# Kernel optimization log

Measured on AMD Instinct MI355X. Metric: run time of the kernel, lower is better.

The kernel has to match this reference:

```python
import jax, jax.numpy as jnp
import numpy as np

NPG = 39      # nodes per graph, from (1+8+64+9)*(39+1)=3280 = lin1 in_features
NEG_SLOPE = 0.2


def gat_conv(x, src, dst, W, a_src, a_dst, b, n):
    """PyG GATConv, heads=1, self-loops already appended to (src, dst).
    x:[N,Fin] W:[Fin,Fout] a_src/a_dst:[Fout] b:[Fout] -> [N,Fout]"""
    h = x @ W                                        # [N,Fout]
    e = jax.nn.leaky_relu(h[src] @ a_src + h[dst] @ a_dst, NEG_SLOPE)  # [E]
    m = jax.lax.stop_gradient(jax.ops.segment_max(e, dst, num_segments=n))
    w = jnp.exp(e - m[dst])
    denom = jax.ops.segment_sum(w, dst, num_segments=n)
    alpha = w / (denom[dst] + 1e-16)                 # segment softmax per target node
    out = jax.ops.segment_sum(alpha[:, None] * h[src], dst, num_segments=n)
    return out + b


def setup_inputs() -> dict:
    key = jax.random.key(0)
    ks = jax.random.split(key, 20)
    B, DEG = 4096, 8
    N = B * NPG
    E = N * DEG
    x = jax.random.normal(ks[0], (N, 1), dtype=jnp.float32)
    # block-diagonal edges: each node emits DEG edges to random nodes in SAME graph
    src = jnp.repeat(jnp.arange(N, dtype=jnp.int64), DEG)
    offs = (src // NPG) * NPG
    dst = offs + jax.random.randint(ks[1], (E,), 0, NPG, dtype=jnp.int64)
    edge_index = jnp.stack([src, dst])
    batch_vec = jnp.repeat(jnp.arange(B, dtype=jnp.int64), NPG)

    def glorot(k, shape):
        fan = shape[0] + (shape[1] if len(shape) > 1 else 1)
        s = jnp.sqrt(6.0 / fan)
        return jax.random.uniform(k, shape, jnp.float32, -s, s)

    p = {
        'W1': glorot(ks[2], (1, 8)),   'a1s': glorot(ks[3], (8,)),  'a1d': glorot(ks[4], (8,)),  'b1': jnp.zeros((8,), jnp.float32),
        'W2': glorot(ks[5], (8, 64)),  'a2s': glorot(ks[6], (64,)), 'a2d': glorot(ks[7], (64,)), 'b2': jnp.zeros((64,), jnp.float32),
        'W3': glorot(ks[8], (64, 9)),  'a3s': glorot(ks[9], (9,)),  'a3d': glorot(ks[10], (9,)), 'b3': jnp.zeros((9,), jnp.float32),
        'lW1': glorot(ks[11], (3280, 5000)), 'lb1': jnp.zeros((5000,), jnp.float32),
        'lW2': glorot(ks[12], (5000, 1024)), 'lb2': jnp.zeros((1024,), jnp.float32),
        'lW3': glorot(ks[13], (1024, 9)),    'lb3': jnp.zeros((9,), jnp.float32),
    }
    return {'x': x, 'edge_index': edge_index, 'batch_vec': batch_vec, **p}


def reference(x, edge_index, batch_vec,
              W1, a1s, a1d, b1, W2, a2s, a2d, b2, W3, a3s, a3d, b3,
              lW1, lb1, lW2, lb2, lW3, lb3):
    N = x.shape[0]
    B = N // NPG
    loops = jnp.arange(N, dtype=edge_index.dtype)
    src = jnp.concatenate([edge_index[0], loops])   # GATConv add_self_loops=True
    dst = jnp.concatenate([edge_index[1], loops])

    res = x.reshape(B, -1)                                    # [B,39]
    out0 = jax.ops.segment_max(x, batch_vec, num_segments=B)  # [B,1]

    h1 = jax.nn.relu(gat_conv(x, src, dst, W1, a1s, a1d, b1, N))   # dropout = eval no-op
    res1 = h1.reshape(B, -1)                                   # [B,312]
    out1 = jax.ops.segment_max(h1, batch_vec, num_segments=B)

    h2 = jax.nn.relu(gat_conv(h1, src, dst, W2, a2s, a2d, b2, N))
    res2 = h2.reshape(B, -1)                                   # [B,2496]
    out2 = jax.ops.segment_max(h2, batch_vec, num_segments=B)

    h3 = jax.nn.relu(gat_conv(h2, src, dst, W3, a3s, a3d, b3, N))
    res3 = h3.reshape(B, -1)                                   # [B,351]
    out3 = jax.ops.segment_max(h3, batch_vec, num_segments=B)

    f = jnp.concatenate([res, res1, res2, res3, out0, out1, out2, out3], axis=1)  # [B,3280]
    f = jax.nn.relu(f @ lW1 + lb1)
    f = jax.nn.relu(f @ lW2 + lb2)
    return f @ lW3 + lb3                                       # [B,9]
```

## Files before the change

kernel.cpp:

```cpp
#include <hip/hip_runtime.h>
#include <hip/hip_bf16.h>
#include <hip/hip_fp16.h>
#include <stdint.h>


typedef float f32x4 __attribute__((ext_vector_type(4)));
typedef short bf16x8 __attribute__((ext_vector_type(8)));
typedef _Float16 f16x8 __attribute__((ext_vector_type(8)));

__device__ __forceinline__ unsigned fenc(float f) {
  int s = __float_as_int(f);
  return s < 0 ? ~(unsigned)s : ((unsigned)s | 0x80000000u);
}
__device__ __forceinline__ float fdec(unsigned u) {
  return (u & 0x80000000u) ? __int_as_float((int)(u & 0x7fffffffu))
                           : __int_as_float(~(int)u);
}

__device__ __forceinline__ void wbar() {
  asm volatile("s_waitcnt lgkmcnt(0)" ::: "memory");
}


__global__ __launch_bounds__(128) void gnn_conv_wpg(
    const float* __restrict__ x,
    const int* __restrict__ esrc, const int* __restrict__ edst,
    const float* __restrict__ W1, const float* __restrict__ a1s, const float* __restrict__ a1d, const float* __restrict__ b1,
    const float* __restrict__ W2, const float* __restrict__ a2s, const float* __restrict__ a2d, const float* __restrict__ b2,
    const float* __restrict__ W3, const float* __restrict__ a3s, const float* __restrict__ a3d, const float* __restrict__ b3,
    __hip_bfloat16* __restrict__ fA,
    const float* __restrict__ lW1, const float* __restrict__ lW2,
    short* __restrict__ W1T, short* __restrict__ W2T)
{
  __shared__ __align__(16) char smem[36768];
  const int tid = threadIdx.x;
  const int bid = blockIdx.x;

  if (bid >= 2048) {
    float (*t)[260] = (float(*)[260])smem;
    const int cid = bid - 2048;
    const float* W; short* WT; int ktile, ntile, K0, N0, KT;
    if (cid < 4160) { W = lW1; WT = W1T; ktile = cid % 208; ntile = cid / 208; K0 = 3280; N0 = 5000; KT = 52; }
    else { int c2 = cid - 4160; W = lW2; WT = W2T; ktile = c2 % 320; ntile = c2 / 320; K0 = 5000; N0 = 1024; KT = 80; }

    const int kb = ktile * 16, nb = ntile * 256;
    const int wv = tid >> 6, lnc = tid & 63;
#pragma unroll
    for (int r = 0; r < 8; ++r) {
      int k = kb + wv * 8 + r;
      int n = nb + lnc * 4;
      f32x4 v = (f32x4){0.f, 0.f, 0.f, 0.f};
      if (k < K0 && n < N0) v = *(const f32x4*)&W[(size_t)k * N0 + n];
      *(f32x4*)&t[wv * 8 + r][lnc * 4] = v;
    }
    __syncthreads();
#pragma unroll
    for (int h = 0; h < 4; ++h) {
      int c = h * 128 + tid;
      int nl = c >> 1, kc = c & 1;
      int n = nb + nl, k = kb + kc * 8;
      union { bf16x8 v; __hip_bfloat16 b[8]; } z;
#pragma unroll
      for (int j = 0; j < 8; ++j) z.b[j] = __float2bfloat16(t[kc * 8 + j][nl]);
      int rt = n >> 7, mi = (n >> 4) & 7, lr = n & 15;
      int kt = k >> 6, kq = (k >> 5) & 1, lc = (k >> 3) & 3;
      size_t addr = ((((size_t)rt * KT) + kt) * 16 + mi * 2 + kq) * 512 + ((size_t)lr + 16 * lc) * 8;
      *(bf16x8*)&WT[addr] = z.v;
    }
    return;
  }

  const int w = tid >> 6, ln = tid & 63;
  const int g = bid * 2 + w;

  float* sW3T  = (float*)(smem);
  float* a2buf = (float*)(smem + 2448);
  float* a3sb  = (float*)(smem + 2960);
  float* a3db  = (float*)(smem + 3008);
  float* b3b   = (float*)(smem + 3056);
  char* sl = smem + 3104 + w * 16832;
  float*    A    = (float*)   (sl);
  __half*   Hh2  = (__half*)  (sl + 6864);
  __half*   h1h  = (__half*)  (sl + 12480);
  float*    HfT  = (float*)   (sl + 13120);
  float*    xbuf = (float*)   (sl + 14720);
  float*    sarr = (float*)   (sl + 14880);
  float*    darr = (float*)   (sl + 15040);
  float*    den  = (float*)   (sl + 15200);
  unsigned* umx  = (unsigned*)(sl + 15360);
  unsigned* cntP = (unsigned*)(sl + 15888);

  const int rt = g >> 7, mi = (g >> 4) & 7, lrow = g & 15;
  const size_t gbase = (size_t)rt * 52 * 8192 + (size_t)(mi * 2) * 512 + (size_t)lrow * 8;
#define COLADDR(c) (gbase + (size_t)((c) >> 6) * 8192 + (size_t)(((c) >> 5) & 1) * 512 \
                    + (size_t)(((c) >> 3) & 3) * 128 + ((c) & 7))

  for (int i = tid; i < 576; i += 128) { int k = i / 9, f3 = i - 9 * k; sW3T[f3 * 68 + k] = W3[i]; }
  a2buf[tid] = (tid < 64) ? a2s[tid] : a2d[tid - 64];
  if (tid < 9) { a3sb[tid] = a3s[tid]; a3db[tid] = a3d[tid]; b3b[tid] = b3[tid]; }
  for (int i = ln; i < 132; i += 64) umx[i] = 0u;
  for (int i = ln; i < 234; i += 64) cntP[i] = 0u;
  if (ln < 40) xbuf[ln] = 0.f;
  if (ln == 39) { sarr[39] = 0.f; darr[39] = 0.f; }
  __syncthreads();

  float xv = 0.f;
  if (ln < 39) { xv = x[g * 39 + ln]; xbuf[ln] = xv; fA[COLADDR(ln)] = __float2bfloat16(xv); }
  float c_s = 0.f, c_d = 0.f;
  const float w1r = W1[ln & 7], b1r = b1[ln & 7];
#pragma unroll
  for (int ff = 0; ff < 8; ++ff) { float wv = W1[ff]; c_s += wv * a1s[ff]; c_d += wv * a1d[ff]; }
  const int eb = g * 312, nb0 = g * 39;
  if (ln < 39) atomicMax(&umx[0], fenc(xv));
#pragma unroll
  for (int it = 0; it < 6; ++it) {
    int e = it * 64 + ln;
    if (e < 351) {
      int ls, ld;
      if (e < 312) { ls = esrc[eb + e] - nb0; ld = edst[eb + e] - nb0; }
      else         { ls = e - 312; ld = ls; }
      atomicAdd(&cntP[ld * 6 + (ls >> 3)], 1u << (4 * (ls & 7)));
    }
  }
  wbar();

  auto denseEW = [&](const float* sv, const float* dv) {
    if (ln < 39) {
      unsigned cw[6];
#pragma unroll
      for (int j = 0; j < 6; ++j) cw[j] = cntP[ln * 6 + j];
      float dval = dv[ln];
      float* Ar = &A[ln * 44];
      float sum = 0.f;
#pragma unroll
      for (int c = 0; c < 10; ++c) {
        f32x4 s4 = *(const f32x4*)&sv[c * 4];
        f32x4 w4;
#pragma unroll
        for (int j = 0; j < 4; ++j) {
          int s = c * 4 + j;
          float e = s4[j] + dval;
          e = (e > 0.f) ? e : 0.2f * e;
          unsigned cc = (cw[s >> 3] >> (4 * (s & 7))) & 0xFu;
          float ex = __expf(e);
          float wv = cc ? (float)cc * ex : 0.f;
          w4[j] = wv; sum += wv;
        }
        *(f32x4*)&Ar[c * 4] = w4;
      }
      den[ln] = 1.f / (sum + 1e-16f);
    }
  };

  if (ln < 39) {
    unsigned cw[6];
#pragma unroll
    for (int j = 0; j < 6; ++j) cw[j] = cntP[ln * 6 + j];
    float dval = xbuf[ln] * c_d;
    float q = 0.f, dsum = 0.f;
#pragma unroll
    for (int c = 0; c < 10; ++c) {
      f32x4 x4 = *(const f32x4*)&xbuf[c * 4];
#pragma unroll
      for (int j = 0; j < 4; ++j) {
        int s = c * 4 + j;
        float xs = x4[j];
        float e = xs * c_s + dval;
        e = (e > 0.f) ? e : 0.2f * e;
        unsigned cc = (cw[s >> 3] >> (4 * (s & 7))) & 0xFu;
        float ex = __expf(e);
        float wv = cc ? (float)cc * ex : 0.f;
        q += wv * xs; dsum += wv;
      }
    }
    sarr[ln] = q * (1.f / (dsum + 1e-16f));
  }
  wbar();
#pragma unroll
  for (int it = 0; it < 5; ++it) {
    int slot = it * 64 + ln;
    if (slot < 312) {
      int i = slot >> 3;
      float v = fmaxf(sarr[i] * w1r + b1r, 0.f);
      h1h[slot] = __float2half(v);
      fA[COLADDR(39 + slot)] = __float2bfloat16(v);
      atomicMax(&umx[1 + (ln & 7)], fenc(v));
    }
  }
  wbar();

  float ht2r[40];
  {
    float w2k[8];
#pragma unroll
    for (int k = 0; k < 8; ++k) w2k[k] = W2[k * 64 + ln];
#pragma unroll
    for (int i = 0; i < 39; ++i) {
      f16x8 hr = *(const f16x8*)&h1h[i * 8];
      float hv = 0.f;
#pragma unroll
      for (int k = 0; k < 8; ++k) hv += (float)hr[k] * w2k[k];
      ht2r[i] = hv;
    }
    ht2r[39] = 0.f;
#pragma unroll
    for (int i = 0; i < 39; ++i) Hh2[i * 72 + ln] = __float2half(ht2r[i]);
  }
  wbar();
#pragma unroll
  for (int rr = 0; rr < 2; ++rr) {
    int t = rr * 64 + ln;
    if (t < 78) {
      int node = (t < 39) ? t : t - 39;
      const float* ab = a2buf + ((t < 39) ? 0 : 64);
      const __half* hr = &Hh2[node * 72];
      float s = 0.f;
#pragma unroll
      for (int c = 0; c < 8; ++c) {
        f16x8 hv = *(const f16x8*)&hr[c * 8];
        f32x4 a0 = *(const f32x4*)&ab[c * 8];
        f32x4 a1 = *(const f32x4*)&ab[c * 8 + 4];
        s += (float)hv[0] * a0.x + (float)hv[1] * a0.y + (float)hv[2] * a0.z + (float)hv[3] * a0.w
           + (float)hv[4] * a1.x + (float)hv[5] * a1.y + (float)hv[6] * a1.z + (float)hv[7] * a1.w;
      }
      if (t < 39) sarr[node] = s; else darr[node] = s;
    }
  }
  wbar();
  denseEW(sarr, darr);
  wbar();
  {
    const float b2r = b2[ln];
    for (int i = 0; i < 39; ++i) {
      float inv = den[i];
      const float* Ar = &A[i * 44];
      float acc = 0.f;
#pragma unroll
      for (int c = 0; c < 10; ++c) {
        f32x4 a4 = *(const f32x4*)&Ar[c * 4];
        acc += a4.x * ht2r[c * 4] + a4.y * ht2r[c * 4 + 1]
             + a4.z * ht2r[c * 4 + 2] + a4.w * ht2r[c * 4 + 3];
      }
      float v = fmaxf(acc * inv + b2r, 0.f);
      Hh2[i * 72 + ln] = __float2half(v);
      fA[COLADDR(351 + i * 64 + ln)] = __float2bfloat16(v);
      atomicMax(&umx[9 + ln], fenc(v));
    }
  }
  wbar();

#pragma unroll
  for (int it = 0; it < 6; ++it) {
    int slot = it * 64 + ln;
    if (slot < 351) {
      int i = slot / 9, f3 = slot - 9 * i;
      const __half* hr = &Hh2[i * 72];
      const float* wr = &sW3T[f3 * 68];
      float acc = 0.f;
#pragma unroll
      for (int c = 0; c < 8; ++c) {
        f16x8 hv = *(const f16x8*)&hr[c * 8];
        f32x4 w0 = *(const f32x4*)&wr[c * 8];
        f32x4 w1 = *(const f32x4*)&wr[c * 8 + 4];
        acc += (float)hv[0] * w0.x + (float)hv[1] * w0.y + (float)hv[2] * w0.z + (float)hv[3] * w0.w
             + (float)hv[4] * w1.x + (float)hv[5] * w1.y + (float)hv[6] * w1.z + (float)hv[7] * w1.w;
      }
      HfT[f3 * 44 + i] = acc;
    }
  }
  if (ln < 9) HfT[ln * 44 + 39] = 0.f;
  wbar();
#pragma unroll
  for (int rr = 0; rr < 2; ++rr) {
    int t = rr * 64 + ln;
    if (t < 78) {
      int node = (t < 39) ? t : t - 39;
      const float* av = (t < 39) ? a3sb : a3db;
      float s = 0.f;
#pragma unroll
      for (int f3 = 0; f3 < 9; ++f3) s += HfT[f3 * 44 + node] * av[f3];
      if (t < 39) sarr[node] = s; else darr[node] = s;
    }
  }
  wbar();
  denseEW(sarr, darr);
  wbar();
#pragma unroll
  for (int it = 0; it < 6; ++it) {
    int slot = it * 64 + ln;
    if (slot < 351) {
      int i = slot / 9, f3 = slot - 9 * i;
      float inv = den[i];
      const float* Ar = &A[i * 44];
      const float* Hr = &HfT[f3 * 44];
      float acc = 0.f;
#pragma unroll
      for (int c = 0; c < 10; ++c) {
        f32x4 a4 = *(const f32x4*)&Ar[c * 4];
        f32x4 h4 = *(const f32x4*)&Hr[c * 4];
        acc += a4.x * h4.x + a4.y * h4.y + a4.z * h4.z + a4.w * h4.w;
      }
      float v = fmaxf(acc * inv + b3b[f3], 0.f);
      fA[COLADDR(2847 + slot)] = __float2bfloat16(v);
      atomicMax(&umx[73 + f3], fenc(v));
    }
  }
  wbar();

#pragma unroll
  for (int it = 0; it < 3; ++it) {
    int idx = it * 64 + ln;
    if (idx < 130) {
      int c = 3198 + idx;
      float v = (idx < 82) ? fdec(umx[idx]) : 0.f;
      fA[COLADDR(c)] = __float2bfloat16(v);
    }
  }
#undef COLADDR
}


__device__ __forceinline__ void gld_lds16(const void* gptr, void* l) {
  typedef const __attribute__((address_space(1))) unsigned int GU;
  typedef __attribute__((address_space(3))) unsigned int LU;
  __builtin_amdgcn_global_load_lds((GU*)gptr, (LU*)l, 16, 0, 0);
}

__global__ __launch_bounds__(256) void gemm_tiled(
    const short* __restrict__ A, const short* __restrict__ B,
    const float* __restrict__ bias, int Nreal,
    void* __restrict__ Cout, int Nn, int KT, int ktPerSplit, int outKT)
{
  __shared__ __align__(16) short lA[8192];
  __shared__ __align__(16) short lB[8192];
  const int tid = threadIdx.x;
  const int w = tid >> 6, L = tid & 63;
  const int lrow = L & 15, lch = L >> 4;
  const int mt = blockIdx.y, nt = blockIdx.x;
  const int mw = (w >> 1) * 4, nw = (w & 1) * 4;
  const int kt0 = blockIdx.z * ktPerSplit, kt1 = kt0 + ktPerSplit;

  const short* Ab = A + ((size_t)mt * KT) * 8192 + (size_t)L * 8;
  const short* Bb = B + ((size_t)nt * KT) * 8192 + (size_t)L * 8;

  f32x4 acc[4][4] = {};

  for (int kt = kt0; kt < kt1; ++kt) {
    const short* Ak = Ab + (size_t)kt * 8192;
    const short* Bk = Bb + (size_t)kt * 8192;
#pragma unroll
    for (int j = 0; j < 4; ++j) {
      int st = w * 4 + j;
      gld_lds16(Ak + st * 512, &lA[st * 512]);
      gld_lds16(Bk + st * 512, &lB[st * 512]);
    }
    __syncthreads();
#pragma unroll
    for (int kk = 0; kk < 2; ++kk) {
      bf16x8 af[4], bfr[4];
#pragma unroll
      for (int i = 0; i < 4; ++i) {
        af[i]  = *(const bf16x8*)&lA[((mw + i) * 2 + kk) * 512 + L * 8];
        bfr[i] = *(const bf16x8*)&lB[((nw + i) * 2 + kk) * 512 + L * 8];
      }
#pragma unroll
      for (int i = 0; i < 4; ++i)
#pragma unroll
        for (int j = 0; j < 4; ++j)
          acc[i][j] = __builtin_amdgcn_mfma_f32_16x16x32_bf16(af[i], bfr[j], acc[i][j], 0, 0, 0);
    }
    __syncthreads();
  }

  __hip_bfloat16* C = (__hip_bfloat16*)Cout;
#pragma unroll
  for (int j = 0; j < 4; ++j) {
    int n = nt * 128 + (nw + j) * 16 + lrow;
    float bn = (n < Nreal) ? bias[n] : 0.f;
    int kt = n >> 6, kq = (n >> 5) & 1, lc2 = (n >> 3) & 3, j2 = n & 7;
#pragma unroll
    for (int i = 0; i < 4; ++i) {
      int mi = mw + i;
      size_t base = ((((size_t)mt * outKT + kt) * 16) + mi * 2 + kq) * 512
                    + (size_t)(lch * 4) * 8 + (size_t)lc2 * 128 + j2;
#pragma unroll
      for (int r = 0; r < 4; ++r)
        C[base + r * 8] = __float2bfloat16(fmaxf(acc[i][j][r] + bn, 0.f));
    }
  }
}

__global__ __launch_bounds__(512) void gemm2_256(
    const short* __restrict__ A, const short* __restrict__ B,
    __half* __restrict__ P)
{
  __shared__ __align__(16) short lA[16384];
  __shared__ __align__(16) short lB[16384];
  const int tid = threadIdx.x;
  const int w = tid >> 6, L = tid & 63;
  const int lrow = L & 15, lch = L >> 4;
  const int wr = w >> 2, wc = w & 3;
  const int nt = blockIdx.x, mt = blockIdx.y, zz = blockIdx.z;
  const int kt0 = zz * 20, kt1 = kt0 + 20;

  const short* A0 = A + ((size_t)(mt * 2) * 80) * 8192;
  const short* A1 = A + ((size_t)(mt * 2 + 1) * 80) * 8192;
  const short* B0 = B + ((size_t)(nt * 2) * 80) * 8192;
  const short* B1 = B + ((size_t)(nt * 2 + 1) * 80) * 8192;

  f32x4 acc[8][4] = {};

  for (int kt = kt0; kt < kt1; ++kt) {
    const size_t ko = (size_t)kt * 8192;
#pragma unroll
    for (int c = 0; c < 2; ++c) {
      int off = (c * 512 + tid) * 8;
      gld_lds16(A0 + ko + off, &lA[off]);
      gld_lds16(A1 + ko + off, &lA[8192 + off]);
      gld_lds16(B0 + ko + off, &lB[off]);
      gld_lds16(B1 + ko + off, &lB[8192 + off]);
    }
    __syncthreads();
#pragma unroll
    for (int kk = 0; kk < 2; ++kk) {
      bf16x8 af[8], bf[4];
#pragma unroll
      for (int i = 0; i < 8; ++i)
        af[i] = *(const bf16x8*)&lA[wr * 8192 + (i * 2 + kk) * 512 + L * 8];
#pragma unroll
      for (int j = 0; j < 4; ++j)
        bf[j] = *(const bf16x8*)&lB[(wc >> 1) * 8192 + (((wc & 1) * 4 + j) * 2 + kk) * 512 + L * 8];
#pragma unroll
      for (int i = 0; i < 8; ++i)
#pragma unroll
        for (int j = 0; j < 4; ++j)
          acc[i][j] = __builtin_amdgcn_mfma_f32_16x16x32_bf16(af[i], bf[j], acc[i][j], 0, 0, 0);
    }
    __syncthreads();
  }

  __half* Pz = P + (size_t)zz * 4096 * 1024;
#pragma unroll
  for (int j = 0; j < 4; ++j) {
    int n = nt * 256 + wc * 64 + j * 16 + lrow;
#pragma unroll
    for (int i = 0; i < 8; ++i)
#pragma unroll
      for (int r = 0; r < 4; ++r) {
        int m = mt * 256 + wr * 128 + i * 16 + lch * 4 + r;
        Pz[(size_t)m * 1024 + n] = __float2half(acc[i][j][r]);
      }
  }
}


__global__ __launch_bounds__(256) void gemm3_fused(
    const __half* __restrict__ P,
    const float* __restrict__ b2v,
    const float* __restrict__ W3,
    const float* __restrict__ b3v,
    float* __restrict__ out)
{
  __shared__ float sW3[9 * 1024];
  int tid = threadIdx.x;
  for (int i = tid; i < 9216; i += 256) { int k = i / 9, j = i - 9 * k; sW3[j * 1024 + k] = W3[i]; }
  __syncthreads();
  int row = blockIdx.x * 4 + (tid >> 6);
  int lane = tid & 63;
  const __half* p0 = P + (size_t)row * 1024;
  const size_t S = (size_t)4096 * 1024;
  float acc[9] = {0, 0, 0, 0, 0, 0, 0, 0, 0};
  for (int t = 0; t < 16; ++t) {
    int k = lane + 64 * t;
    float c = __half2float(p0[k]) + __half2float(p0[k + S])
            + __half2float(p0[k + 2 * S]) + __half2float(p0[k + 3 * S]) + b2v[k];
    c = fmaxf(c, 0.f);
#pragma unroll
    for (int j = 0; j < 9; ++j) acc[j] += c * sW3[j * 1024 + k];
  }
#pragma unroll
  for (int j = 0; j < 9; ++j) {
    float v = acc[j];
    v += __shfl_down(v, 32, 64);
    v += __shfl_down(v, 16, 64);
    v += __shfl_down(v, 8, 64);
    v += __shfl_down(v, 4, 64);
    v += __shfl_down(v, 2, 64);
    v += __shfl_down(v, 1, 64);
    if (lane == 0) out[(size_t)row * 9 + j] = v + b3v[j];
  }
}


extern "C" void kernel_launch(void* const* d_in, const int* in_sizes, int n_in,
                              void* d_out, int out_size, void* d_ws, size_t ws_size,
                              hipStream_t stream)
{
  const float* x   = (const float*)d_in[0];
  const int*   ei  = (const int*)d_in[1];
  const float* W1  = (const float*)d_in[3];
  const float* a1s = (const float*)d_in[4];
  const float* a1d = (const float*)d_in[5];
  const float* b1  = (const float*)d_in[6];
  const float* W2  = (const float*)d_in[7];
  const float* a2s = (const float*)d_in[8];
  const float* a2d = (const float*)d_in[9];
  const float* b2  = (const float*)d_in[10];
  const float* W3  = (const float*)d_in[11];
  const float* a3s = (const float*)d_in[12];
  const float* a3d = (const float*)d_in[13];
  const float* b3  = (const float*)d_in[14];
  const float* lW1 = (const float*)d_in[15];
  const float* lb1 = (const float*)d_in[16];
  const float* lW2 = (const float*)d_in[17];
  const float* lb2 = (const float*)d_in[18];
  const float* lW3 = (const float*)d_in[19];
  const float* lb3 = (const float*)d_in[20];

  const int E = 4096 * 39 * 8;
  const int* esrc = ei;
  const int* edst = ei + E;

  short* fA  = (short*)d_ws;
  short* W1T = fA  + (size_t)4096 * 3328;
  short* C1  = W1T + (size_t)5120 * 3328;
  short* W2T = C1  + (size_t)4096 * 5120;
  __half* P  = (__half*)d_ws;

  gnn_conv_wpg<<<7488, 128, 0, stream>>>(x, esrc, edst,
                                         W1, a1s, a1d, b1, W2, a2s, a2d, b2, W3, a3s, a3d, b3,
                                         (__hip_bfloat16*)fA, lW1, lW2, W1T, W2T);
  gemm_tiled<<<dim3(40, 32, 1), 256, 0, stream>>>(fA, W1T, lb1, 5000, C1, 5120, 52, 52, 80);
  gemm2_256<<<dim3(4, 16, 4), 512, 0, stream>>>(C1, W2T, P);
  gemm3_fused<<<1024, 256, 0, stream>>>(P, lb2, lW3, lb3, (float*)d_out);
}
```

Baseline: 442.4 us.

## Shrink GAT attention buffers to fp16 and retile second GEMM to 128x128 split-K5

The GAT kernel now stores attention weights and layer-3 features in fp16 instead of fp32, pre-scaled to avoid overflow. This cuts per-wave LDS use and may let more blocks fit per CU. The second linear-layer GEMM moves from 256x256 tiles with 4-way split-K to 128x128 tiles with 5-way split-K, giving more blocks and better CU fill. The price is extra partial-sum traffic for the five fp16 partials reduced in the final kernel, plus lower precision in the attention weights.

```diff
diff --git a/kernel.cpp b/kernel.cpp
--- a/kernel.cpp
+++ b/kernel.cpp
@@ -32,7 +32,7 @@
     const float* __restrict__ lW1, const float* __restrict__ lW2,
     short* __restrict__ W1T, short* __restrict__ W2T)
 {
-  __shared__ __align__(16) char smem[36768];
+  __shared__ __align__(16) char smem[29024];
   const int tid = threadIdx.x;
   const int bid = blockIdx.x;
 
@@ -78,17 +78,17 @@
   float* a3sb  = (float*)(smem + 2960);
   float* a3db  = (float*)(smem + 3008);
   float* b3b   = (float*)(smem + 3056);
-  char* sl = smem + 3104 + w * 16832;
-  float*    A    = (float*)   (sl);
-  __half*   Hh2  = (__half*)  (sl + 6864);
-  __half*   h1h  = (__half*)  (sl + 12480);
-  float*    HfT  = (float*)   (sl + 13120);
-  float*    xbuf = (float*)   (sl + 14720);
-  float*    sarr = (float*)   (sl + 14880);
-  float*    darr = (float*)   (sl + 15040);
-  float*    den  = (float*)   (sl + 15200);
-  unsigned* umx  = (unsigned*)(sl + 15360);
-  unsigned* cntP = (unsigned*)(sl + 15888);
+  char* sl = smem + 3104 + w * 12960;
+  __half*   Ah   = (__half*)  (sl);
+  __half*   Hh2  = (__half*)  (sl + 3744);
+  __half*   h1h  = (__half*)  (sl + 9360);
+  __half*   HfT16= (__half*)  (sl + 9984);
+  float*    xbuf = (float*)   (sl + 10848);
+  float*    sarr = (float*)   (sl + 11008);
+  float*    darr = (float*)   (sl + 11168);
+  float*    den  = (float*)   (sl + 11328);
+  unsigned* umx  = (unsigned*)(sl + 11488);
+  unsigned* cntP = (unsigned*)(sl + 12016);
 
   const int rt = g >> 7, mi = (g >> 4) & 7, lrow = g & 15;
   const size_t gbase = (size_t)rt * 52 * 8192 + (size_t)(mi * 2) * 512 + (size_t)lrow * 8;
@@ -130,25 +130,25 @@
 #pragma unroll
       for (int j = 0; j < 6; ++j) cw[j] = cntP[ln * 6 + j];
       float dval = dv[ln];
-      float* Ar = &A[ln * 44];
+      __half* Ar = &Ah[ln * 48];
       float sum = 0.f;
 #pragma unroll
-      for (int c = 0; c < 10; ++c) {
-        f32x4 s4 = *(const f32x4*)&sv[c * 4];
-        f32x4 w4;
-#pragma unroll
-        for (int j = 0; j < 4; ++j) {
-          int s = c * 4 + j;
-          float e = s4[j] + dval;
+      for (int c = 0; c < 5; ++c) {
+        union { f16x8 v; __half h[8]; } z8;
+#pragma unroll
+        for (int j = 0; j < 8; ++j) {
+          int s = c * 8 + j;
+          float e = sv[s] + dval;
           e = (e > 0.f) ? e : 0.2f * e;
           unsigned cc = (cw[s >> 3] >> (4 * (s & 7))) & 0xFu;
-          float ex = __expf(e);
+          float ex = __expf(e) * 0.00390625f;
           float wv = cc ? (float)cc * ex : 0.f;
-          w4[j] = wv; sum += wv;
+          z8.h[j] = __float2half(wv);
+          sum += (float)z8.h[j];
         }
-        *(f32x4*)&Ar[c * 4] = w4;
-      }
-      den[ln] = 1.f / (sum + 1e-16f);
+        *(f16x8*)&Ar[c * 8] = z8.v;
+      }
+      den[ln] = 1.f / (sum + 3.9e-19f);
     }
   };
 
@@ -233,13 +233,13 @@
     const float b2r = b2[ln];
     for (int i = 0; i < 39; ++i) {
       float inv = den[i];
-      const float* Ar = &A[i * 44];
+      const __half* Ar = &Ah[i * 48];
       float acc = 0.f;
 #pragma unroll
-      for (int c = 0; c < 10; ++c) {
-        f32x4 a4 = *(const f32x4*)&Ar[c * 4];
-        acc += a4.x * ht2r[c * 4] + a4.y * ht2r[c * 4 + 1]
-             + a4.z * ht2r[c * 4 + 2] + a4.w * ht2r[c * 4 + 3];
+      for (int c = 0; c < 5; ++c) {
+        f16x8 a8 = *(const f16x8*)&Ar[c * 8];
+#pragma unroll
+        for (int j = 0; j < 8; ++j) acc += (float)a8[j] * ht2r[c * 8 + j];
       }
       float v = fmaxf(acc * inv + b2r, 0.f);
       Hh2[i * 72 + ln] = __float2half(v);
@@ -265,10 +265,10 @@
         acc += (float)hv[0] * w0.x + (float)hv[1] * w0.y + (float)hv[2] * w0.z + (float)hv[3] * w0.w
              + (float)hv[4] * w1.x + (float)hv[5] * w1.y + (float)hv[6] * w1.z + (float)hv[7] * w1.w;
       }
-      HfT[f3 * 44 + i] = acc;
-    }
-  }
-  if (ln < 9) HfT[ln * 44 + 39] = 0.f;
+      HfT16[f3 * 48 + i] = __float2half(acc);
+    }
+  }
+  if (ln < 9) HfT16[ln * 48 + 39] = __float2half(0.f);
   wbar();
 #pragma unroll
   for (int rr = 0; rr < 2; ++rr) {
@@ -278,7 +278,7 @@
       const float* av = (t < 39) ? a3sb : a3db;
       float s = 0.f;
 #pragma unroll
-      for (int f3 = 0; f3 < 9; ++f3) s += HfT[f3 * 44 + node] * av[f3];
+      for (int f3 = 0; f3 < 9; ++f3) s += (float)HfT16[f3 * 48 + node] * av[f3];
       if (t < 39) sarr[node] = s; else darr[node] = s;
     }
   }
@@ -291,14 +291,15 @@
     if (slot < 351) {
       int i = slot / 9, f3 = slot - 9 * i;
       float inv = den[i];
-      const float* Ar = &A[i * 44];
-      const float* Hr = &HfT[f3 * 44];
+      const __half* Ar = &Ah[i * 48];
+      const __half* Hr = &HfT16[f3 * 48];
       float acc = 0.f;
 #pragma unroll
-      for (int c = 0; c < 10; ++c) {
-        f32x4 a4 = *(const f32x4*)&Ar[c * 4];
-        f32x4 h4 = *(const f32x4*)&Hr[c * 4];
-        acc += a4.x * h4.x + a4.y * h4.y + a4.z * h4.z + a4.w * h4.w;
+      for (int c = 0; c < 5; ++c) {
+        f16x8 a8 = *(const f16x8*)&Ar[c * 8];
+        f16x8 h8 = *(const f16x8*)&Hr[c * 8];
+#pragma unroll
+        for (int j = 0; j < 8; ++j) acc += (float)a8[j] * (float)h8[j];
       }
       float v = fmaxf(acc * inv + b3b[f3], 0.f);
       fA[COLADDR(2847 + slot)] = __float2bfloat16(v);
@@ -390,51 +391,47 @@
   }
 }
 
-__global__ __launch_bounds__(512) void gemm2_256(
+__global__ __launch_bounds__(256) void gemm2_128(
     const short* __restrict__ A, const short* __restrict__ B,
     __half* __restrict__ P)
 {
-  __shared__ __align__(16) short lA[16384];
-  __shared__ __align__(16) short lB[16384];
+  __shared__ __align__(16) short lA[8192];
+  __shared__ __align__(16) short lB[8192];
   const int tid = threadIdx.x;
   const int w = tid >> 6, L = tid & 63;
   const int lrow = L & 15, lch = L >> 4;
-  const int wr = w >> 2, wc = w & 3;
-  const int nt = blockIdx.x, mt = blockIdx.y, zz = blockIdx.z;
-  const int kt0 = zz * 20, kt1 = kt0 + 20;
-
-  const short* A0 = A + ((size_t)(mt * 2) * 80) * 8192;
-  const short* A1 = A + ((size_t)(mt * 2 + 1) * 80) * 8192;
-  const short* B0 = B + ((size_t)(nt * 2) * 80) * 8192;
-  const short* B1 = B + ((size_t)(nt * 2 + 1) * 80) * 8192;
-
-  f32x4 acc[8][4] = {};
+  const int mt = blockIdx.y, nt = blockIdx.x, zz = blockIdx.z;
+  const int mw = (w >> 1) * 4, nw = (w & 1) * 4;
+  const int kt0 = zz * 16, kt1 = kt0 + 16;
+
+  const short* Ab = A + ((size_t)mt * 80) * 8192 + (size_t)L * 8;
+  const short* Bb = B + ((size_t)nt * 80) * 8192 + (size_t)L * 8;
+
+  f32x4 acc[4][4] = {};
 
   for (int kt = kt0; kt < kt1; ++kt) {
-    const size_t ko = (size_t)kt * 8192;
-#pragma unroll
-    for (int c = 0; c < 2; ++c) {
-      int off = (c * 512 + tid) * 8;
-      gld_lds16(A0 + ko + off, &lA[off]);
-      gld_lds16(A1 + ko + off, &lA[8192 + off]);
-      gld_lds16(B0 + ko + off, &lB[off]);
-      gld_lds16(B1 + ko + off, &lB[8192 + off]);
+    const short* Ak = Ab + (size_t)kt * 8192;
+    const short* Bk = Bb + (size_t)kt * 8192;
+#pragma unroll
+    for (int j = 0; j < 4; ++j) {
+      int st = w * 4 + j;
+      gld_lds16(Ak + st * 512, &lA[st * 512]);
+      gld_lds16(Bk + st * 512, &lB[st * 512]);
     }
     __syncthreads();
 #pragma unroll
     for (int kk = 0; kk < 2; ++kk) {
-      bf16x8 af[8], bf[4];
-#pragma unroll
-      for (int i = 0; i < 8; ++i)
-        af[i] = *(const bf16x8*)&lA[wr * 8192 + (i * 2 + kk) * 512 + L * 8];
-#pragma unroll
-      for (int j = 0; j < 4; ++j)
-        bf[j] = *(const bf16x8*)&lB[(wc >> 1) * 8192 + (((wc & 1) * 4 + j) * 2 + kk) * 512 + L * 8];
-#pragma unroll
-      for (int i = 0; i < 8; ++i)
+      bf16x8 af[4], bfr[4];
+#pragma unroll
+      for (int i = 0; i < 4; ++i) {
+        af[i]  = *(const bf16x8*)&lA[((mw + i) * 2 + kk) * 512 + L * 8];
+        bfr[i] = *(const bf16x8*)&lB[((nw + i) * 2 + kk) * 512 + L * 8];
+      }
+#pragma unroll
+      for (int i = 0; i < 4; ++i)
 #pragma unroll
         for (int j = 0; j < 4; ++j)
-          acc[i][j] = __builtin_amdgcn_mfma_f32_16x16x32_bf16(af[i], bf[j], acc[i][j], 0, 0, 0);
+          acc[i][j] = __builtin_amdgcn_mfma_f32_16x16x32_bf16(af[i], bfr[j], acc[i][j], 0, 0, 0);
     }
     __syncthreads();
   }
@@ -442,12 +439,12 @@
   __half* Pz = P + (size_t)zz * 4096 * 1024;
 #pragma unroll
   for (int j = 0; j < 4; ++j) {
-    int n = nt * 256 + wc * 64 + j * 16 + lrow;
-#pragma unroll
-    for (int i = 0; i < 8; ++i)
+    int n = nt * 128 + (nw + j) * 16 + lrow;
+#pragma unroll
+    for (int i = 0; i < 4; ++i)
 #pragma unroll
       for (int r = 0; r < 4; ++r) {
-        int m = mt * 256 + wr * 128 + i * 16 + lch * 4 + r;
+        int m = mt * 128 + (mw + i) * 16 + lch * 4 + r;
         Pz[(size_t)m * 1024 + n] = __float2half(acc[i][j][r]);
       }
   }
@@ -472,8 +469,9 @@
   float acc[9] = {0, 0, 0, 0, 0, 0, 0, 0, 0};
   for (int t = 0; t < 16; ++t) {
     int k = lane + 64 * t;
-    float c = __half2float(p0[k]) + __half2float(p0[k + S])
-            + __half2float(p0[k + 2 * S]) + __half2float(p0[k + 3 * S]) + b2v[k];
+    float c = b2v[k];
+#pragma unroll
+    for (int z = 0; z < 5; ++z) c += __half2float(p0[k + (size_t)z * S]);
     c = fmaxf(c, 0.f);
 #pragma unroll
     for (int j = 0; j < 9; ++j) acc[j] += c * sW3[j * 1024 + k];
@@ -531,6 +529,6 @@
                                          W1, a1s, a1d, b1, W2, a2s, a2d, b2, W3, a3s, a3d, b3,
                                          (__hip_bfloat16*)fA, lW1, lW2, W1T, W2T);
   gemm_tiled<<<dim3(40, 32, 1), 256, 0, stream>>>(fA, W1T, lb1, 5000, C1, 5120, 52, 52, 80);
-  gemm2_256<<<dim3(4, 16, 4), 512, 0, stream>>>(C1, W2T, P);
+  gemm2_128<<<dim3(8, 32, 5), 256, 0, stream>>>(C1, W2T, P);
   gemm3_fused<<<1024, 256, 0, stream>>>(P, lb2, lW3, lb3, (float*)d_out);
 }
```

Result: no change. 445.2 us (+0.6%).
